# Performance work log

Measured on AMD Instinct MI355X. Metric: run time of the kernel, lower is better.

Reference implementation:

```python
import jax, jax.numpy as jnp
import numpy as np

H = 4096        # hidden_size
NH = 32         # num_attention_heads
NKV = 8         # num_key_value_heads
HD = H // NH    # head_dim = 128
N_REP = NH // NKV
SCALE = HD ** -0.5


def _rope(x, cos, sin):
    # x: (B, h, S, HD); cos/sin: (S, HD//2) broadcast over batch/heads
    x1 = x[..., 0::2]
    x2 = x[..., 1::2]
    return jnp.concatenate([x1 * cos - x2 * sin, x1 * sin + x2 * cos], axis=-1)


def setup_inputs() -> dict:
    key = jax.random.key(0)
    ks = jax.random.split(key, 9)
    B, S = 2, 2048
    return {
        "hidden_states": jax.random.normal(ks[0], (B, S, H), jnp.float32),
        "cos": jax.random.uniform(ks[1], (S, HD // 2), jnp.float32),
        "sin": jax.random.uniform(ks[2], (S, HD // 2), jnp.float32),
        "Wq": jax.random.normal(ks[3], (H, H), jnp.float32) * (H ** -0.5),
        "Wk": jax.random.normal(ks[4], (NKV * HD, H), jnp.float32) * (H ** -0.5),
        "bk": jax.random.normal(ks[5], (NKV * HD,), jnp.float32) * 0.01,
        "Wv": jax.random.normal(ks[6], (NKV * HD, H), jnp.float32) * (H ** -0.5),
        "bv": jax.random.normal(ks[7], (NKV * HD,), jnp.float32) * 0.01,
        "Wo": jax.random.normal(ks[8], (H, H), jnp.float32) * (H ** -0.5),
    }


def reference(hidden_states, cos, sin, Wq, Wk, bk, Wv, bv, Wo):
    B, S, _ = hidden_states.shape
    # projections (torch Linear: x @ W.T + b)
    q = (hidden_states @ Wq.T).reshape(B, S, NH, HD).transpose(0, 2, 1, 3)
    k = (hidden_states @ Wk.T + bk).reshape(B, S, NKV, HD).transpose(0, 2, 1, 3)
    v = (hidden_states @ Wv.T + bv).reshape(B, S, NKV, HD).transpose(0, 2, 1, 3)
    q = _rope(q, cos, sin)
    k = _rope(k, cos, sin)
    # GQA repeat_kv: (B, NKV, S, HD) -> (B, NH, S, HD)
    k = jnp.repeat(k, N_REP, axis=1)
    v = jnp.repeat(v, N_REP, axis=1)
    # full attention (no mask is actually applied in the source forward)
    scores = jnp.einsum('bhqd,bhkd->bhqk', q, k) * SCALE
    attn = jax.nn.softmax(scores, axis=-1)
    out = jnp.einsum('bhqk,bhkd->bhqd', attn, v)
    out = out.transpose(0, 2, 1, 3).reshape(B, S, H)
    return out @ Wo.T
```

## Files before the change

### kernel.cpp

```cpp
#include <hip/hip_runtime.h>

typedef unsigned short u16;
typedef short short8 __attribute__((ext_vector_type(8)));
typedef float floatx4 __attribute__((ext_vector_type(4)));

#define H_ 4096
#define NH_ 32
#define NKV_ 8
#define HD_ 128
#define SEQ_ 2048
#define BATCH_ 2
#define ROWS_ (BATCH_*SEQ_)
#define KVW_ (NKV_*HD_)
#define NQKV_ (H_ + 2*KVW_)
#define VSTRIDE_ NQKV_
#define SCALE_ 0.08838834764831845f
#define TSCALE_ (SCALE_*1.442695040888963f)

__device__ __forceinline__ u16 f2bf(float f) {
  union { float f; unsigned u; } x; x.f = f;
  unsigned r = x.u + 0x7fffu + ((x.u >> 16) & 1u);
  return (u16)(r >> 16);
}
__device__ __forceinline__ float bf2f(u16 h) {
  union { unsigned u; float f; } x; x.u = ((unsigned)h) << 16;
  return x.f;
}
__device__ __forceinline__ unsigned cvt_pk_bf16(float lo, float hi) {
  unsigned r;
  asm("v_cvt_pk_bf16_f32 %0, %1, %2" : "=v"(r) : "v"(lo), "v"(hi));
  return r;
}

__global__ __launch_bounds__(256) void cvt_all(const float* __restrict__ hs, const float* __restrict__ Wq,
                                               const float* __restrict__ Wk, const float* __restrict__ Wv,
                                               const float* __restrict__ Wo,
                                               u16* __restrict__ hs_bf, u16* __restrict__ Wqkv_bf,
                                               u16* __restrict__ Wo_bf) {
  const int n_hs = ROWS_*H_/4;
  const int n_wq = H_*H_/4;
  const int n_wk = KVW_*H_/4;
  const long total = (long)n_hs + n_wq + 2*(long)n_wk + n_wq;
  for (long i = (long)blockIdx.x*256 + threadIdx.x; i < total; i += (long)gridDim.x*256) {
    const float* s; u16* d; long j = i;
    if (j < n_hs)                       { s = hs; d = hs_bf; }
    else if ((j -= n_hs) < n_wq)        { s = Wq; d = Wqkv_bf; }
    else if ((j -= n_wq) < n_wk)        { s = Wk; d = Wqkv_bf + (size_t)H_*H_; }
    else if ((j -= n_wk) < n_wk)        { s = Wv; d = Wqkv_bf + (size_t)(H_+KVW_)*H_; }
    else { j -= n_wk;                     s = Wo; d = Wo_bf; }
    float4 v = ((const float4*)s)[j];
    ushort4 o; o.x = f2bf(v.x); o.y = f2bf(v.y); o.z = f2bf(v.z); o.w = f2bf(v.w);
    ((ushort4*)d)[j] = o;
  }
}

__global__ __launch_bounds__(256) void bias_concat(const float* __restrict__ bk,
                                                   const float* __restrict__ bv,
                                                   float* __restrict__ dst) {
  int i = blockIdx.x * 256 + threadIdx.x;
  if (i >= NQKV_) return;
  float v = 0.f;
  if (i >= H_ + KVW_)      v = bv[i - (H_ + KVW_)];
  else if (i >= H_)        v = bk[i - H_];
  dst[i] = v;
}

template<int BF16_OUT, int HAS_BIAS>
__global__ __launch_bounds__(512, 2) void gemm_nt_8p(const u16* __restrict__ A, const u16* __restrict__ B,
                                                     const float* __restrict__ bias, void* __restrict__ Cout,
                                                     int M, int N, int K)
{
  __shared__ __align__(16) u16 lds[65536];
  char* ldsB = (char*)lds;
  const int tid  = threadIdx.x;
  const int lane = tid & 63;
  const int wave = tid >> 6;
  const int ln   = lane & 15;
  const int quad = lane >> 4;
  const int wm   = wave >> 2;
  const int wn   = wave & 3;

  const int xcd = blockIdx.x & 7;
  const int k_  = blockIdx.x >> 3;
  const int m0  = ((xcd >> 2) * 8 + (k_ & 7)) * 256;
  const int n0  = ((xcd & 3) * 4 + (k_ >> 3)) * 256;

  const u16* srcp[4][2];
  {
    int ob0 = wave*2048 + lane*16;
#pragma unroll
    for (int h = 0; h < 4; ++h) {
#pragma unroll
      for (int j = 0; j < 2; ++j) {
        int ob  = ob0 + j*1024;
        int row = ob >> 6;
        int sl  = ((ob >> 4) & 3) ^ ((row >> 1) & 3);
        int kst = h >> 1;
        if ((h & 1) == 0) srcp[h][j] = A + (size_t)(m0 + row)*K + kst*32 + sl*8;
        else              srcp[h][j] = B + (size_t)(n0 + row)*K + kst*32 + sl*8;
      }
    }
  }

#define STAGE(h_, p_, kt_)                                                          \
  {                                                                                 \
    __builtin_amdgcn_global_load_lds(                                               \
      (const __attribute__((address_space(1))) void*)(srcp[h_][0] + (kt_)*64),      \
      (__attribute__((address_space(3))) void*)(ldsB + (((h_)&1)*65536 + (p_)*32768 \
          + ((h_)>>1)*16384 + wave*2048)), 16, 0, 0);                               \
    __builtin_amdgcn_global_load_lds(                                               \
      (const __attribute__((address_space(1))) void*)(srcp[h_][1] + (kt_)*64),      \
      (__attribute__((address_space(3))) void*)(ldsB + (((h_)&1)*65536 + (p_)*32768 \
          + ((h_)>>1)*16384 + wave*2048 + 1024)), 16, 0, 0);                        \
  }

  const int slq16 = (quad ^ ((ln >> 1) & 3)) * 16;
  const int aoffL = (wm*128 + ln)*64 + slq16;
  const int boffL = (wn*64  + ln)*64 + slq16;

  floatx4 zf = {0.f, 0.f, 0.f, 0.f};
  floatx4 acc[8][4];
#pragma unroll
  for (int i = 0; i < 8; ++i)
#pragma unroll
    for (int j = 0; j < 4; ++j) acc[i][j] = zf;

  STAGE(0, 0, 0) STAGE(1, 0, 0) STAGE(2, 0, 0) STAGE(3, 0, 0)
  asm volatile("s_waitcnt vmcnt(4)");
  __builtin_amdgcn_s_barrier();

  const int NT = K >> 6;
  for (int t = 0; t < NT; ++t) {
    const int p  = t & 1;
    const int np = p ^ 1;
    const char* ab = ldsB + p*32768;
    const char* bb = ldsB + 65536 + p*32768;
    short8 af[4], bq[4];

#pragma unroll
    for (int j = 0; j < 4; ++j) bq[j] = *(const short8*)(bb + boffL + j*1024);
#pragma unroll
    for (int i = 0; i < 4; ++i) af[i] = *(const short8*)(ab + aoffL + i*1024);
    if (t + 1 < NT) { STAGE(0, np, t+1) STAGE(1, np, t+1) }
    __builtin_amdgcn_s_barrier();
    asm volatile("s_waitcnt lgkmcnt(0)");
    __builtin_amdgcn_sched_barrier(0);
    __builtin_amdgcn_s_setprio(1);
#pragma unroll
    for (int i = 0; i < 4; ++i)
#pragma unroll
      for (int j = 0; j < 4; ++j)
        acc[i][j] = __builtin_amdgcn_mfma_f32_16x16x32_bf16(af[i], bq[j], acc[i][j], 0, 0, 0);
    __builtin_amdgcn_s_setprio(0);
    __builtin_amdgcn_s_barrier();

#pragma unroll
    for (int i = 0; i < 4; ++i) af[i] = *(const short8*)(ab + aoffL + (4+i)*1024);
    __builtin_amdgcn_s_barrier();
    asm volatile("s_waitcnt lgkmcnt(0)");
    __builtin_amdgcn_sched_barrier(0);
    __builtin_amdgcn_s_setprio(1);
#pragma unroll
    for (int i = 0; i < 4; ++i)
#pragma unroll
      for (int j = 0; j < 4; ++j)
        acc[4+i][j] = __builtin_amdgcn_mfma_f32_16x16x32_bf16(af[i], bq[j], acc[4+i][j], 0, 0, 0);
    __builtin_amdgcn_s_setprio(0);
    if (t + 1 < NT) { asm volatile("s_waitcnt vmcnt(4)"); }
    else            { asm volatile("s_waitcnt vmcnt(0)"); }
    __builtin_amdgcn_s_barrier();

#pragma unroll
    for (int j = 0; j < 4; ++j) bq[j] = *(const short8*)(bb + 16384 + boffL + j*1024);
#pragma unroll
    for (int i = 0; i < 4; ++i) af[i] = *(const short8*)(ab + 16384 + aoffL + i*1024);
    if (t + 1 < NT) { STAGE(2, np, t+1) STAGE(3, np, t+1) }
    __builtin_amdgcn_s_barrier();
    asm volatile("s_waitcnt lgkmcnt(0)");
    __builtin_amdgcn_sched_barrier(0);
    __builtin_amdgcn_s_setprio(1);
#pragma unroll
    for (int i = 0; i < 4; ++i)
#pragma unroll
      for (int j = 0; j < 4; ++j)
        acc[i][j] = __builtin_amdgcn_mfma_f32_16x16x32_bf16(af[i], bq[j], acc[i][j], 0, 0, 0);
    __builtin_amdgcn_s_setprio(0);
    __builtin_amdgcn_s_barrier();

#pragma unroll
    for (int i = 0; i < 4; ++i) af[i] = *(const short8*)(ab + 16384 + aoffL + (4+i)*1024);
    __builtin_amdgcn_s_barrier();
    asm volatile("s_waitcnt lgkmcnt(0)");
    __builtin_amdgcn_sched_barrier(0);
    __builtin_amdgcn_s_setprio(1);
#pragma unroll
    for (int i = 0; i < 4; ++i)
#pragma unroll
      for (int j = 0; j < 4; ++j)
        acc[4+i][j] = __builtin_amdgcn_mfma_f32_16x16x32_bf16(af[i], bq[j], acc[4+i][j], 0, 0, 0);
    __builtin_amdgcn_s_setprio(0);
    if (t + 1 < NT) { asm volatile("s_waitcnt vmcnt(4)"); }
    __builtin_amdgcn_s_barrier();
  }
#undef STAGE

#pragma unroll
  for (int i = 0; i < 8; ++i) {
#pragma unroll
    for (int j = 0; j < 4; ++j) {
      int row = m0 + wm*128 + i*16 + quad*4;
      int col = n0 + wn*64  + j*16 + ln;
      float bv_ = HAS_BIAS ? bias[col] : 0.f;
#pragma unroll
      for (int r = 0; r < 4; ++r) {
        float v = acc[i][j][r] + bv_;
        if (BF16_OUT) ((u16*)Cout)[(size_t)(row+r)*N + col] = f2bf(v);
        else          ((float*)Cout)[(size_t)(row+r)*N + col] = v;
      }
    }
  }
}

template<int BF16_OUT, int HAS_BIAS>
__global__ __launch_bounds__(512, 2) void gemm_nt_8p_h(const u16* __restrict__ A, const u16* __restrict__ B,
                                                       const float* __restrict__ bias, void* __restrict__ Cout,
                                                       int M, int N, int K)
{
  __shared__ __align__(16) u16 lds[73728];
  char* ldsB = (char*)lds;
  const int tid  = threadIdx.x;
  const int lane = tid & 63;
  const int wave = tid >> 6;
  const int ln   = lane & 15;
  const int quad = lane >> 4;
  const int wm   = wave >> 2;
  const int wn   = wave & 3;

  const int xcd = blockIdx.x & 7;
  const int w_  = blockIdx.x >> 3;
  const int rnd = w_ >> 5;
  const int wi  = w_ & 31;
  const int m0  = ((xcd >> 1) * 8 + (wi & 7)) * 128;
  const int n0  = (rnd * 8 + (xcd & 1) * 4 + (wi >> 3)) * 256;

  const u16* srcA[2];
  const u16* srcB[2][2];
  {
    int ob  = wave*1024 + lane*16;
    int row = ob >> 6;
    int sl  = ((ob >> 4) & 3) ^ ((row >> 1) & 3);
#pragma unroll
    for (int kst = 0; kst < 2; ++kst)
      srcA[kst] = A + (size_t)(m0 + row)*K + kst*32 + sl*8;
  }
#pragma unroll
  for (int j = 0; j < 2; ++j) {
    int ob  = wave*2048 + j*1024 + lane*16;
    int row = ob >> 6;
    int sl  = ((ob >> 4) & 3) ^ ((row >> 1) & 3);
#pragma unroll
    for (int kst = 0; kst < 2; ++kst)
      srcB[kst][j] = B + (size_t)(n0 + row)*K + kst*32 + sl*8;
  }

#define STAGEH(kst_, p_, kt_)                                                        \
  {                                                                                  \
    __builtin_amdgcn_global_load_lds(                                                \
      (const __attribute__((address_space(1))) void*)(srcA[kst_] + (kt_)*64),        \
      (__attribute__((address_space(3))) void*)(ldsB + ((p_)*16384 + (kst_)*8192     \
          + wave*1024)), 16, 0, 0);                                                  \
    __builtin_amdgcn_global_load_lds(                                                \
      (const __attribute__((address_space(1))) void*)(srcB[kst_][0] + (kt_)*64),     \
      (__attribute__((address_space(3))) void*)(ldsB + (49152 + (p_)*32768           \
          + (kst_)*16384 + wave*2048)), 16, 0, 0);                                   \
    __builtin_amdgcn_global_load_lds(                                                \
      (const __attribute__((address_space(1))) void*)(srcB[kst_][1] + (kt_)*64),     \
      (__attribute__((address_space(3))) void*)(ldsB + (49152 + (p_)*32768           \
          + (kst_)*16384 + wave*2048 + 1024)), 16, 0, 0);                            \
  }

  const int slq16 = (quad ^ ((ln >> 1) & 3)) * 16;
  const int aoffL = (wm*64 + ln)*64 + slq16;
  const int boffL = (wn*64 + ln)*64 + slq16;

  floatx4 zf = {0.f, 0.f, 0.f, 0.f};
  floatx4 acc[4][4];
#pragma unroll
  for (int i = 0; i < 4; ++i)
#pragma unroll
    for (int j = 0; j < 4; ++j) acc[i][j] = zf;

  const int NT = K >> 6;
  STAGEH(0, 0, 0) STAGEH(1, 0, 0)
  if (NT > 1) {
    STAGEH(0, 1, 1) STAGEH(1, 1, 1)
    asm volatile("s_waitcnt vmcnt(9)");
  } else {
    asm volatile("s_waitcnt vmcnt(3)");
  }
  __builtin_amdgcn_s_barrier();

  int par = 0;
  for (int t = 0; t < NT; ++t) {
    const int spar = (par == 0) ? 2 : par - 1;
    const char* ab = ldsB + par*16384;
    const char* bb = ldsB + 49152 + par*32768;
    short8 af[4], bq[4];

#pragma unroll
    for (int j = 0; j < 4; ++j) bq[j] = *(const short8*)(bb + boffL + j*1024);
#pragma unroll
    for (int i = 0; i < 4; ++i) af[i] = *(const short8*)(ab + aoffL + i*1024);
    if (t + 2 < NT) STAGEH(0, spar, t+2)
    __builtin_amdgcn_s_barrier();
    asm volatile("s_waitcnt lgkmcnt(0)");
    __builtin_amdgcn_sched_barrier(0);
    __builtin_amdgcn_s_setprio(1);
#pragma unroll
    for (int i = 0; i < 4; ++i)
#pragma unroll
      for (int j = 0; j < 4; ++j)
        acc[i][j] = __builtin_amdgcn_mfma_f32_16x16x32_bf16(af[i], bq[j], acc[i][j], 0, 0, 0);
    __builtin_amdgcn_s_setprio(0);
    if (t + 2 < NT)      { asm volatile("s_waitcnt vmcnt(9)"); }
    else if (t + 1 < NT) { asm volatile("s_waitcnt vmcnt(6)"); }
    else                 { asm volatile("s_waitcnt vmcnt(0)"); }
    __builtin_amdgcn_s_barrier();

#pragma unroll
    for (int j = 0; j < 4; ++j) bq[j] = *(const short8*)(bb + 16384 + boffL + j*1024);
#pragma unroll
    for (int i = 0; i < 4; ++i) af[i] = *(const short8*)(ab + 8192 + aoffL + i*1024);
    if (t + 2 < NT) STAGEH(1, spar, t+2)
    __builtin_amdgcn_s_barrier();
    asm volatile("s_waitcnt lgkmcnt(0)");
    __builtin_amdgcn_sched_barrier(0);
    __builtin_amdgcn_s_setprio(1);
#pragma unroll
    for (int i = 0; i < 4; ++i)
#pragma unroll
      for (int j = 0; j < 4; ++j)
        acc[i][j] = __builtin_amdgcn_mfma_f32_16x16x32_bf16(af[i], bq[j], acc[i][j], 0, 0, 0);
    __builtin_amdgcn_s_setprio(0);
    if (t + 2 < NT)      { asm volatile("s_waitcnt vmcnt(9)"); }
    else if (t + 1 < NT) { asm volatile("s_waitcnt vmcnt(3)"); }
    __builtin_amdgcn_s_barrier();

    par = (par == 2) ? 0 : par + 1;
  }
#undef STAGEH

#pragma unroll
  for (int i = 0; i < 4; ++i) {
#pragma unroll
    for (int j = 0; j < 4; ++j) {
      int row = m0 + wm*64 + i*16 + quad*4;
      int col = n0 + wn*64 + j*16 + ln;
      float bv_ = HAS_BIAS ? bias[col] : 0.f;
#pragma unroll
      for (int r = 0; r < 4; ++r) {
        float v = acc[i][j][r] + bv_;
        if (BF16_OUT) ((u16*)Cout)[(size_t)(row+r)*N + col] = f2bf(v);
        else          ((float*)Cout)[(size_t)(row+r)*N + col] = v;
      }
    }
  }
}

__global__ __launch_bounds__(256) void rope_kernel(const u16* __restrict__ X, u16* __restrict__ Y,
                                                   const float* __restrict__ cosb, const float* __restrict__ sinb,
                                                   int nheads, int total, int istride, int ostride)
{
  int idx = blockIdx.x * 256 + threadIdx.x;
  if (idx >= total) return;
  int d = idx & 63;
  int t = idx >> 6;
  int hh = t % nheads;
  int row = t / nheads;
  int s = row & (SEQ_ - 1);
  size_t bi = (size_t)row * istride + hh * HD_;
  size_t bo = (size_t)row * ostride + hh * HD_;
  float x1 = bf2f(X[bi + 2*d]);
  float x2 = bf2f(X[bi + 2*d + 1]);
  float c  = cosb[s*64 + d];
  float sn = sinb[s*64 + d];
  Y[bo + d]      = f2bf(x1*c - x2*sn);
  Y[bo + 64 + d] = f2bf(x1*sn + x2*c);
}

#define KS_TILE (64*128)

__global__ __launch_bounds__(512, 2) void attn_fwd(const u16* __restrict__ Q, const u16* __restrict__ K,
                                                   const u16* __restrict__ V, u16* __restrict__ O)
{
  __shared__ __align__(16) u16 Ks[2*KS_TILE];
  __shared__ __align__(16) u16 Vt[128*72];
  const int tid  = threadIdx.x;
  const int lane = tid & 63;
  const int wave = tid >> 6;
  const int ln   = lane & 15;
  const int quad = lane >> 4;
  const int lin = (blockIdx.x & 7) * 64 + (blockIdx.x >> 3);
  const int bh  = lin >> 3;
  const int b   = bh >> 5;
  const int h   = bh & 31;
  const int kvh = h >> 2;
  const int q0  = (lin & 7) * 256;

  short8 qf[2][4];
#pragma unroll
  for (int mt = 0; mt < 2; ++mt) {
    const u16* qbase = Q + (size_t)(b*SEQ_ + q0 + wave*32 + mt*16 + ln) * H_ + h * HD_;
#pragma unroll
    for (int kst = 0; kst < 4; ++kst)
      qf[mt][kst] = *(const short8*)(qbase + kst*32 + quad*8);
  }

  short8 bones;
  {
    short v1 = (ln == 0) ? (short)0x3F80 : (short)0;
#pragma unroll
    for (int j = 0; j < 8; ++j) bones[j] = v1;
  }

  int kou[2];
  const u16* ks0[2];
#pragma unroll
  for (int i = 0; i < 2; ++i) {
    int ou = wave*2048 + i*1024;
    int ob = ou + lane*16;
    int key = ob >> 8;
    int dgp = (ob >> 4) & 15;
    int dgl = dgp ^ (key & 15);
    kou[i] = ou;
    ks0[i] = K + (size_t)(b*SEQ_ + key)*KVW_ + kvh*HD_ + dgl*8;
  }
  const int g  = tid & 15;
  const int dg = (tid >> 4) & 15;
  const int j2 = tid >> 8;
  const u16* vs0 = V + (size_t)(b*SEQ_ + j2*32 + g)*VSTRIDE_ + kvh*HD_ + dg*8;
  const int k0v = ((g >> 1) & 1)*32 + (g >> 2)*8 + (g & 1)*4 + j2*2;

  floatx4 zf = {0.f, 0.f, 0.f, 0.f};
  floatx4 o[2][8];
  floatx4 ol[2];
#pragma unroll
  for (int mt = 0; mt < 2; ++mt) {
    ol[mt] = zf;
#pragma unroll
    for (int jt = 0; jt < 8; ++jt) o[mt][jt] = zf;
  }
  float mrow[2] = {-1e30f, -1e30f};

  int4 vreg[2];
#pragma unroll
  for (int i = 0; i < 2; ++i)
    __builtin_amdgcn_global_load_lds((const __attribute__((address_space(1))) void*)ks0[i],
        (__attribute__((address_space(3))) void*)((char*)Ks + kou[i]), 16, 0, 0);
#pragma unroll
  for (int jj = 0; jj < 2; ++jj)
    vreg[jj] = *(const int4*)(vs0 + (size_t)(jj*16)*VSTRIDE_);
  {
    union { int4 v; u16 u[8]; } w[2];
    w[0].v = vreg[0]; w[1].v = vreg[1];
#pragma unroll
    for (int dd = 0; dd < 8; ++dd) {
      ushort2 t2; t2.x = w[0].u[dd]; t2.y = w[1].u[dd];
      *(ushort2*)&Vt[(dg*8 + dd)*72 + k0v] = t2;
    }
  }
  __syncthreads();

  const int NT = SEQ_ / 64;
  for (int t = 0; t < NT; ++t) {
    if (t + 1 < NT) {
      size_t roff = (size_t)(t+1) * 64 * KVW_;
      char* kb = (char*)Ks + ((t+1)&1) * (KS_TILE*2);
#pragma unroll
      for (int i = 0; i < 2; ++i)
        __builtin_amdgcn_global_load_lds((const __attribute__((address_space(1))) void*)(ks0[i] + roff),
            (__attribute__((address_space(3))) void*)(kb + kou[i]), 16, 0, 0);
      size_t voff = (size_t)(t+1) * 64 * VSTRIDE_;
#pragma unroll
      for (int jj = 0; jj < 2; ++jj)
        vreg[jj] = *(const int4*)(vs0 + voff + (size_t)(jj*16)*VSTRIDE_);
    }
    const u16* Kc = Ks + (t&1)*KS_TILE;

    floatx4 s[2][4];
#pragma unroll
    for (int nt = 0; nt < 4; ++nt) { s[0][nt] = zf; s[1][nt] = zf; }
    __builtin_amdgcn_s_setprio(1);
#pragma unroll
    for (int kst = 0; kst < 4; ++kst) {
      int dgp = (kst*4 + quad) ^ ln;
#pragma unroll
      for (int nt = 0; nt < 4; ++nt) {
        short8 kf = *(const short8*)&Kc[(nt*16 + ln)*128 + dgp*8];
        s[0][nt] = __builtin_amdgcn_mfma_f32_16x16x32_bf16(kf, qf[0][kst], s[0][nt], 0, 0, 0);
        s[1][nt] = __builtin_amdgcn_mfma_f32_16x16x32_bf16(kf, qf[1][kst], s[1][nt], 0, 0, 0);
      }
    }
    __builtin_amdgcn_s_setprio(0);

    float rmv[2];
    bool ok = true;
#pragma unroll
    for (int mt = 0; mt < 2; ++mt) {
      float m0_ = fmaxf(fmaxf(s[mt][0][0], s[mt][0][1]), fmaxf(s[mt][0][2], s[mt][0][3]));
      float m1_ = fmaxf(fmaxf(s[mt][1][0], s[mt][1][1]), fmaxf(s[mt][1][2], s[mt][1][3]));
      float m2_ = fmaxf(fmaxf(s[mt][2][0], s[mt][2][1]), fmaxf(s[mt][2][2], s[mt][2][3]));
      float m3_ = fmaxf(fmaxf(s[mt][3][0], s[mt][3][1]), fmaxf(s[mt][3][2], s[mt][3][3]));
      float rm = fmaxf(fmaxf(m0_, m1_), fmaxf(m2_, m3_)) * TSCALE_;
      rm = fmaxf(rm, __shfl_xor(rm, 16));
      rm = fmaxf(rm, __shfl_xor(rm, 32));
      rmv[mt] = rm;
      ok = ok && (rm - mrow[mt] <= 8.0f);
    }
    if (!__all(ok)) {
#pragma unroll
      for (int mt = 0; mt < 2; ++mt) {
        float mn = fmaxf(mrow[mt], rmv[mt]);
        float al = exp2f(mrow[mt] - mn);
        mrow[mt] = mn;
        float av[4];
#pragma unroll
        for (int r = 0; r < 4; ++r) av[r] = __shfl(al, (lane & 48) | (quad*4 + r));
#pragma unroll
        for (int r = 0; r < 4; ++r) {
          float a_ = av[r];
#pragma unroll
          for (int jt = 0; jt < 8; ++jt) o[mt][jt][r] *= a_;
          ol[mt][r] *= a_;
        }
      }
    }
    short8 pa[2][2];
#pragma unroll
    for (int mt = 0; mt < 2; ++mt) {
      float mn = mrow[mt];
      float p[4][4];
#pragma unroll
      for (int nt = 0; nt < 4; ++nt)
#pragma unroll
        for (int r = 0; r < 4; ++r)
          p[r][nt] = exp2f(fmaf(s[mt][nt][r], TSCALE_, -mn));
#pragma unroll
      for (int k2 = 0; k2 < 2; ++k2) {
        union { unsigned u[4]; short8 v; } pk;
        pk.u[0] = cvt_pk_bf16(p[2*k2][0],   p[2*k2][1]);
        pk.u[1] = cvt_pk_bf16(p[2*k2][2],   p[2*k2][3]);
        pk.u[2] = cvt_pk_bf16(p[2*k2+1][0], p[2*k2+1][1]);
        pk.u[3] = cvt_pk_bf16(p[2*k2+1][2], p[2*k2+1][3]);
        pa[mt][k2] = pk.v;
      }
    }

    __builtin_amdgcn_s_setprio(1);
#pragma unroll
    for (int k2 = 0; k2 < 2; ++k2) {
#pragma unroll
      for (int jt = 0; jt < 8; ++jt) {
        short8 vf = *(const short8*)&Vt[(jt*16 + ln)*72 + k2*32 + quad*8];
        o[0][jt] = __builtin_amdgcn_mfma_f32_16x16x32_bf16(pa[0][k2], vf, o[0][jt], 0, 0, 0);
        o[1][jt] = __builtin_amdgcn_mfma_f32_16x16x32_bf16(pa[1][k2], vf, o[1][jt], 0, 0, 0);
      }
      ol[0] = __builtin_amdgcn_mfma_f32_16x16x32_bf16(pa[0][k2], bones, ol[0], 0, 0, 0);
      ol[1] = __builtin_amdgcn_mfma_f32_16x16x32_bf16(pa[1][k2], bones, ol[1], 0, 0, 0);
    }
    __builtin_amdgcn_s_setprio(0);

    __syncthreads();
    if (t + 1 < NT) {
      union { int4 v; u16 u[8]; } w[2];
      w[0].v = vreg[0]; w[1].v = vreg[1];
#pragma unroll
      for (int dd = 0; dd < 8; ++dd) {
        ushort2 t2; t2.x = w[0].u[dd]; t2.y = w[1].u[dd];
        *(ushort2*)&Vt[(dg*8 + dd)*72 + k0v] = t2;
      }
    }
    __syncthreads();
  }

#pragma unroll
  for (int mt = 0; mt < 2; ++mt) {
#pragma unroll
    for (int r = 0; r < 4; ++r) {
      float lv = __shfl(ol[mt][r], lane & 48);
      float inv = 1.f / lv;
      size_t row = (size_t)(b*SEQ_ + q0 + wave*32 + mt*16 + quad*4 + r);
      u16* dst = O + row * H_ + h * HD_ + ln;
#pragma unroll
      for (int jt = 0; jt < 8; ++jt)
        dst[jt*16] = f2bf(o[mt][jt][r] * inv);
    }
  }
}

extern "C" void kernel_launch(void* const* d_in, const int* in_sizes, int n_in,
                              void* d_out, int out_size, void* d_ws, size_t ws_size,
                              hipStream_t stream) {
  const float* hs   = (const float*)d_in[0];
  const float* cosb = (const float*)d_in[1];
  const float* sinb = (const float*)d_in[2];
  const float* Wq   = (const float*)d_in[3];
  const float* Wk   = (const float*)d_in[4];
  const float* bk   = (const float*)d_in[5];
  const float* Wv   = (const float*)d_in[6];
  const float* bv   = (const float*)d_in[7];
  const float* Wo   = (const float*)d_in[8];
  float* out = (float*)d_out;

  char* ws = (char*)d_ws;
  u16*   hs_bf   = (u16*)(ws +          0);
  u16*   Wqkv_bf = (u16*)(ws +   33554432);
  u16*   Wo_bf   = (u16*)(ws +   83886080);
  u16*   QKV0    = (u16*)(ws +  117440512);
  u16*   Qr      = (u16*)(ws +  167772160);
  u16*   Kr      = (u16*)(ws +  201326592);
  float* biasqkv = (float*)(ws + 209715200);
  u16*   Oa      = hs_bf;

  cvt_all<<<2048, 256, 0, stream>>>(hs, Wq, Wk, Wv, Wo, hs_bf, Wqkv_bf, Wo_bf);
  bias_concat<<<(NQKV_ + 255)/256, 256, 0, stream>>>(bk, bv, biasqkv);

  gemm_nt_8p_h<1,1><<<dim3((ROWS_/128)*(NQKV_/256)), dim3(512), 0, stream>>>(hs_bf, Wqkv_bf, biasqkv, QKV0, ROWS_, NQKV_, H_);
  rope_kernel<<<(ROWS_*NH_*64)/256,  256, 0, stream>>>(QKV0,       Qr, cosb, sinb, NH_,  ROWS_*NH_*64,  NQKV_, H_);
  rope_kernel<<<(ROWS_*NKV_*64)/256, 256, 0, stream>>>(QKV0 + H_,  Kr, cosb, sinb, NKV_, ROWS_*NKV_*64, NQKV_, KVW_);
  attn_fwd<<<dim3(512), dim3(512), 0, stream>>>(Qr, Kr, QKV0 + H_ + KVW_, Oa);
  gemm_nt_8p<0,0><<<dim3((ROWS_/256)*(H_/256)), dim3(512), 0, stream>>>(Oa, Wo_bf, nullptr, out, ROWS_, H_, H_);
}
```

Before: 791.2 us.

## Double-buffer LDS fragment registers to overlap ds_reads with MFMA in GEMM loop

Restructures the GEMM main loop so the register fragments for the next half-tile are loaded from LDS while the MFMAs for the current half-tile run, using two sets of A/B fragment registers. The intent is to hide LDS read latency behind the matrix ops instead of waiting on lgkmcnt before each MFMA block. The vmcnt waits and barrier placement are reworked to match. The extra fragment registers raise register pressure, which could lower occupancy, and the retuned waits must stay correct for the three-stage global-to-LDS pipeline.

```diff
diff --git a/kernel.cpp b/kernel.cpp
--- a/kernel.cpp
+++ b/kernel.cpp
@@ -290,6 +290,8 @@
 #pragma unroll
     for (int j = 0; j < 4; ++j) acc[i][j] = zf;
 
+  short8 aA[4], bA[4], aB[4], bB[4];
+
   const int NT = K >> 6;
   STAGEH(0, 0, 0) STAGEH(1, 0, 0)
   if (NT > 1) {
@@ -299,54 +301,63 @@
     asm volatile("s_waitcnt vmcnt(3)");
   }
   __builtin_amdgcn_s_barrier();
+#pragma unroll
+  for (int j = 0; j < 4; ++j) bA[j] = *(const short8*)(ldsB + 49152 + boffL + j*1024);
+#pragma unroll
+  for (int i = 0; i < 4; ++i) aA[i] = *(const short8*)(ldsB + aoffL + i*1024);
+  asm volatile("s_waitcnt lgkmcnt(0)");
+  __builtin_amdgcn_sched_barrier(0);
 
   int par = 0;
   for (int t = 0; t < NT; ++t) {
-    const int spar = (par == 0) ? 2 : par - 1;
-    const char* ab = ldsB + par*16384;
-    const char* bb = ldsB + 49152 + par*32768;
-    short8 af[4], bq[4];
-
-#pragma unroll
-    for (int j = 0; j < 4; ++j) bq[j] = *(const short8*)(bb + boffL + j*1024);
-#pragma unroll
-    for (int i = 0; i < 4; ++i) af[i] = *(const short8*)(ab + aoffL + i*1024);
-    if (t + 2 < NT) STAGEH(0, spar, t+2)
-    __builtin_amdgcn_s_barrier();
+    const int pn = (par == 2) ? 0 : par + 1;
+    const int ps = (par == 0) ? 2 : par - 1;
+    const char* ab  = ldsB + par*16384;
+    const char* bb  = ldsB + 49152 + par*32768;
+    const char* abn = ldsB + pn*16384;
+    const char* bbn = ldsB + 49152 + pn*32768;
+
+    if (t + 1 < NT) { asm volatile("s_waitcnt vmcnt(6)"); }
+    else            { asm volatile("s_waitcnt vmcnt(0)"); }
+    __builtin_amdgcn_s_barrier();
+#pragma unroll
+    for (int j = 0; j < 4; ++j) bB[j] = *(const short8*)(bb + 16384 + boffL + j*1024);
+#pragma unroll
+    for (int i = 0; i < 4; ++i) aB[i] = *(const short8*)(ab + 8192 + aoffL + i*1024);
+    if (t + 2 < NT) STAGEH(0, ps, t+2)
+    __builtin_amdgcn_sched_barrier(0);
+    __builtin_amdgcn_s_setprio(1);
+#pragma unroll
+    for (int i = 0; i < 4; ++i)
+#pragma unroll
+      for (int j = 0; j < 4; ++j)
+        acc[i][j] = __builtin_amdgcn_mfma_f32_16x16x32_bf16(aA[i], bA[j], acc[i][j], 0, 0, 0);
+    __builtin_amdgcn_s_setprio(0);
     asm volatile("s_waitcnt lgkmcnt(0)");
     __builtin_amdgcn_sched_barrier(0);
+
+    if (t + 2 < NT)      { asm volatile("s_waitcnt vmcnt(6)"); }
+    else if (t + 1 < NT) { asm volatile("s_waitcnt vmcnt(3)"); }
+    __builtin_amdgcn_s_barrier();
+    if (t + 1 < NT) {
+#pragma unroll
+      for (int j = 0; j < 4; ++j) bA[j] = *(const short8*)(bbn + boffL + j*1024);
+#pragma unroll
+      for (int i = 0; i < 4; ++i) aA[i] = *(const short8*)(abn + aoffL + i*1024);
+    }
+    if (t + 2 < NT) STAGEH(1, ps, t+2)
+    __builtin_amdgcn_sched_barrier(0);
     __builtin_amdgcn_s_setprio(1);
 #pragma unroll
     for (int i = 0; i < 4; ++i)
 #pragma unroll
       for (int j = 0; j < 4; ++j)
-        acc[i][j] = __builtin_amdgcn_mfma_f32_16x16x32_bf16(af[i], bq[j], acc[i][j], 0, 0, 0);
-    __builtin_amdgcn_s_setprio(0);
-    if (t + 2 < NT)      { asm volatile("s_waitcnt vmcnt(9)"); }
-    else if (t + 1 < NT) { asm volatile("s_waitcnt vmcnt(6)"); }
-    else                 { asm volatile("s_waitcnt vmcnt(0)"); }
-    __builtin_amdgcn_s_barrier();
-
-#pragma unroll
-    for (int j = 0; j < 4; ++j) bq[j] = *(const short8*)(bb + 16384 + boffL + j*1024);
-#pragma unroll
-    for (int i = 0; i < 4; ++i) af[i] = *(const short8*)(ab + 8192 + aoffL + i*1024);
-    if (t + 2 < NT) STAGEH(1, spar, t+2)
-    __builtin_amdgcn_s_barrier();
+        acc[i][j] = __builtin_amdgcn_mfma_f32_16x16x32_bf16(aB[i], bB[j], acc[i][j], 0, 0, 0);
+    __builtin_amdgcn_s_setprio(0);
     asm volatile("s_waitcnt lgkmcnt(0)");
     __builtin_amdgcn_sched_barrier(0);
-    __builtin_amdgcn_s_setprio(1);
-#pragma unroll
-    for (int i = 0; i < 4; ++i)
-#pragma unroll
-      for (int j = 0; j < 4; ++j)
-        acc[i][j] = __builtin_amdgcn_mfma_f32_16x16x32_bf16(af[i], bq[j], acc[i][j], 0, 0, 0);
-    __builtin_amdgcn_s_setprio(0);
-    if (t + 2 < NT)      { asm volatile("s_waitcnt vmcnt(9)"); }
-    else if (t + 1 < NT) { asm volatile("s_waitcnt vmcnt(3)"); }
-    __builtin_amdgcn_s_barrier();
-
-    par = (par == 2) ? 0 : par + 1;
+
+    par = pn;
   }
 #undef STAGEH
 
```

Result: no change. 788.7 us (-0.3%).
